# Performance work log

Measured on AMD Instinct MI355X. Metric: run time of the kernel, lower is better.

The kernel has to match this reference:

```python
import jax, jax.numpy as jnp
import numpy as np

NUM_HEADS = 16
NUM_FEATURES = 1024
HEAD_DIM = NUM_FEATURES // NUM_HEADS
B, S = 2, 2048


def setup_inputs() -> dict:
    key = jax.random.key(0)
    ks = jax.random.split(key, 12)
    d = NUM_FEATURES
    scale = 1.0 / np.sqrt(d)
    inp = {
        'q': jax.random.normal(ks[0], (B, S, d), jnp.float32),
        'v': jax.random.normal(ks[1], (B, S, d), jnp.float32),
        'k': jax.random.normal(ks[2], (B, S, d), jnp.float32),
        'mask': jnp.ones((1, 1, S, S), jnp.float32),
        # Dense params: flax kernel layout (in, out)
        'Wq': jax.random.normal(ks[3], (d, d), jnp.float32) * scale,
        'bq': jnp.zeros((d,), jnp.float32),
        'Wv': jax.random.normal(ks[4], (d, d), jnp.float32) * scale,
        'bv': jnp.zeros((d,), jnp.float32),
        'Wk': jax.random.normal(ks[5], (d, d), jnp.float32) * scale,
        'bk': jnp.zeros((d,), jnp.float32),
        'Wo': jax.random.normal(ks[6], (d, d), jnp.float32) * scale,
        'bo': jnp.zeros((d,), jnp.float32),
    }
    return inp


def _split_heads(x):
    b, s, _ = x.shape
    return jnp.transpose(x.reshape(b, s, NUM_HEADS, HEAD_DIM), (0, 2, 1, 3))  # [B,H,S,Dh]


def reference(q, v, k, mask, Wq, bq, Wv, bv, Wk, bk, Wo, bo):
    q = q @ Wq + bq
    v = v @ Wv + bv
    k = k @ Wk + bk
    qh = _split_heads(q) / jnp.sqrt(jnp.float32(NUM_FEATURES))  # note: sqrt(d_model), as in source
    kh = _split_heads(k)
    vh = _split_heads(v)
    logits = jnp.einsum('bhqd,bhkd->bhqk', qh, kh)
    logits = logits - 1e9 * (1.0 - mask)
    weights = jax.nn.softmax(logits, axis=-1)
    # dropout deterministic (eval_mode=True) -> identity
    out = jnp.einsum('bhqk,bhkd->bhqd', weights, vh)
    out = jnp.transpose(out, (0, 2, 1, 3)).reshape(q.shape[0], q.shape[1], NUM_FEATURES)
    return out @ Wo + bo
```

## Files before the change

kernel.cpp:

```cpp
#include <hip/hip_runtime.h>
#include <hip/hip_bf16.h>


namespace {
constexpr int DM = 1024;
constexpr int NH = 16;
constexpr int HD = 64;
constexpr int SQ = 2048;
constexpr int M_TOT = 2 * SQ;
constexpr int NT = SQ / 64;

using f32x4  = __attribute__((ext_vector_type(4))) float;
using f32x16 = __attribute__((ext_vector_type(16))) float;
using bf16x8 = __attribute__((ext_vector_type(8))) short;
using u16 = unsigned short;

__device__ __forceinline__ u16 f2bf(float f) {
  union { float f; unsigned u; } x; x.f = f;
  unsigned r = x.u + 0x7fffu + ((x.u >> 16) & 1u);
  return (u16)(r >> 16);
}

__device__ __forceinline__ unsigned pk2(float lo, float hi) {
  unsigned r;
  asm("v_cvt_pk_bf16_f32 %0, %1, %2" : "=v"(r) : "v"(lo), "v"(hi));
  return r;
}

__device__ __forceinline__ float fexp2(float x) {
  float r;
  asm("v_exp_f32 %0, %1" : "=v"(r) : "v"(x));
  return r;
}

__device__ __forceinline__ f32x16 mfma32(bf16x8 a, bf16x8 b, f32x16 c) {
  return __builtin_amdgcn_mfma_f32_32x32x16_bf16(a, b, c, 0, 0, 0);
}

__device__ __forceinline__ void gld16(const void* g, void* l) {
  __builtin_amdgcn_global_load_lds((const __attribute__((address_space(1))) void*)g,
                                   (__attribute__((address_space(3))) void*)l, 16, 0, 0);
}
}

__global__ __launch_bounds__(256) void tobf_kernel(const float* __restrict__ q,
                                                   const float* __restrict__ k,
                                                   const float* __restrict__ v,
                                                   u16* __restrict__ out) {
  const float* src = blockIdx.y == 0 ? q : (blockIdx.y == 1 ? k : v);
  u16* dst = out + (size_t)blockIdx.y * M_TOT * DM;
  size_t i = ((size_t)blockIdx.x * 256 + threadIdx.x) * 8;
  float4 a = *(const float4*)(src + i), b = *(const float4*)(src + i + 4);
  union { u16 us[8]; uint4 v4; } pk;
  pk.us[0] = f2bf(a.x); pk.us[1] = f2bf(a.y); pk.us[2] = f2bf(a.z); pk.us[3] = f2bf(a.w);
  pk.us[4] = f2bf(b.x); pk.us[5] = f2bf(b.y); pk.us[6] = f2bf(b.z); pk.us[7] = f2bf(b.w);
  *(uint4*)(dst + i) = pk.v4;
}

__global__ __launch_bounds__(256) void wtrans_kernel(const float* __restrict__ W,
                                                     u16* __restrict__ Wt) {
  __shared__ u16 tile[64][65];
  const int t = threadIdx.x;
  const int k0 = blockIdx.y * 64, n0 = blockIdx.x * 64;
#pragma unroll
  for (int i = 0; i < 16; ++i) {
    int flat = t + i * 256;
    int kk = flat >> 6, nn = flat & 63;
    tile[kk][nn] = f2bf(W[(size_t)(k0 + kk) * DM + n0 + nn]);
  }
  __syncthreads();
#pragma unroll
  for (int i = 0; i < 16; ++i) {
    int flat = t + i * 256;
    int nn = flat >> 6, kk = flat & 63;
    Wt[(size_t)(n0 + nn) * DM + k0 + kk] = tile[kk][nn];
  }
}

__global__ __launch_bounds__(256) void vtrans_kernel(const u16* __restrict__ Vh,
                                                     u16* __restrict__ Vt) {
  __shared__ u16 tile[64][80];
  const int s0 = blockIdx.x * 64, bh = blockIdx.y;
  const u16* src = Vh + ((size_t)bh * SQ + s0) * HD;
  u16* dst = Vt + (size_t)bh * HD * SQ + s0;
  const int t = threadIdx.x;
#pragma unroll
  for (int i = 0; i < 2; ++i) {
    int flat = t + i * 256;
    int sr = flat >> 3, ch = flat & 7;
    *(uint4*)&tile[sr][ch * 8] = *(const uint4*)&src[(size_t)sr * HD + ch * 8];
  }
  __syncthreads();
#pragma unroll
  for (int i = 0; i < 2; ++i) {
    int flat = t + i * 256;
    int dh = flat >> 3, ch = flat & 7;
    union { u16 us[8]; uint2 h[2]; } pk;
#pragma unroll
    for (int j = 0; j < 8; ++j) pk.us[j] = tile[ch * 8 + j][dh];
#pragma unroll
    for (int kq = 0; kq < 2; ++kq) {
      int g = ch * 2 + kq;
      int gl = (g & ~3) | ((g & 1) << 1) | ((g & 2) >> 1);
      *(uint2*)&dst[(size_t)dh * SQ + gl * 4] = pk.h[kq];
    }
  }
}

template <int EPI>
__device__ __forceinline__ void gemm_core(const u16* __restrict__ A,
                                          const u16* __restrict__ Wt,
                                          const float* __restrict__ bias,
                                          void* __restrict__ C, float scale,
                                          int m0, int n0, u16* ldsA, u16* ldsB) {
  const int t = threadIdx.x;
  const int lane = t & 63, w = t >> 6;
  const int wm = w >> 1, wn = w & 1;
  const int c = lane & 15, g = lane >> 4;
  const int lr = lane >> 3, lc = lane & 7;
  f32x4 acc[2][4] = {};

  for (int k0 = 0; k0 < DM; k0 += 64) {
    __syncthreads();
#pragma unroll
    for (int j = 0; j < 2; ++j) {
      int row = w * 16 + j * 8 + lr;
      int gc = lc ^ (row & 7);
      gld16(&A[(size_t)(m0 + row) * DM + k0 + gc * 8], (char*)ldsA + w * 2048 + j * 1024);
    }
#pragma unroll
    for (int j = 0; j < 4; ++j) {
      int row = w * 32 + j * 8 + lr;
      int gc = lc ^ (row & 7);
      gld16(&Wt[(size_t)(n0 + row) * DM + k0 + gc * 8], (char*)ldsB + w * 4096 + j * 1024);
    }
    __syncthreads();
#pragma unroll
    for (int ks = 0; ks < 2; ++ks) {
      bf16x8 af[2], bfr[4];
#pragma unroll
      for (int mi = 0; mi < 2; ++mi) {
        int R = wm * 32 + mi * 16 + c;
        af[mi] = *(const bf16x8*)((const char*)ldsA + R * 128 + ((4 * ks + g) ^ (R & 7)) * 16);
      }
#pragma unroll
      for (int ni = 0; ni < 4; ++ni) {
        int R = wn * 64 + ni * 16 + c;
        bfr[ni] = *(const bf16x8*)((const char*)ldsB + R * 128 + ((4 * ks + g) ^ (R & 7)) * 16);
      }
#pragma unroll
      for (int mi = 0; mi < 2; ++mi)
#pragma unroll
        for (int ni = 0; ni < 4; ++ni)
          acc[mi][ni] =
              __builtin_amdgcn_mfma_f32_16x16x32_bf16(af[mi], bfr[ni], acc[mi][ni], 0, 0, 0);
    }
  }
  float bv_[4];
#pragma unroll
  for (int ni = 0; ni < 4; ++ni) bv_[ni] = bias[n0 + wn * 64 + ni * 16 + c];
#pragma unroll
  for (int mi = 0; mi < 2; ++mi)
#pragma unroll
    for (int ni = 0; ni < 4; ++ni)
#pragma unroll
      for (int r = 0; r < 4; ++r) {
        int m = m0 + wm * 32 + mi * 16 + g * 4 + r;
        int n = n0 + wn * 64 + ni * 16 + c;
        float val = acc[mi][ni][r] + bv_[ni];
        if (EPI == 2) {
          ((float*)C)[(size_t)m * DM + n] = val;
        } else {
          int b = m >> 11, s = m & (SQ - 1);
          int h = n >> 6, dh = n & (HD - 1);
          ((u16*)C)[((size_t)(b * NH + h) * SQ + s) * HD + dh] = f2bf(val * scale);
        }
      }
}

__global__ __launch_bounds__(256) void qkvgemm_kernel(const u16* __restrict__ QKVbf,
                                                      const u16* __restrict__ W3t,
                                                      const float* __restrict__ bq,
                                                      const float* __restrict__ bk,
                                                      const float* __restrict__ bv,
                                                      u16* __restrict__ Qh,
                                                      u16* __restrict__ Kh,
                                                      u16* __restrict__ Vh) {
  __shared__ __align__(16) u16 ldsA[64 * 64];
  __shared__ __align__(16) u16 ldsB[128 * 64];
  int bid = blockIdx.x;
  int swz = (bid & 7) * 192 + (bid >> 3);
  int which = swz >> 9;
  int sub = swz & 511;
  int mt = sub >> 3, nt = sub & 7;
  const u16* A = QKVbf + (size_t)which * M_TOT * DM;
  const u16* Wt = W3t + (size_t)which * DM * DM;
  const float* bias = which == 0 ? bq : (which == 1 ? bk : bv);
  u16* C = which == 0 ? Qh : (which == 1 ? Kh : Vh);
  float scale = which == 0 ? 0.045084222f : 1.0f;
  gemm_core<0>(A, Wt, bias, C, scale, mt * 64, nt * 128, ldsA, ldsB);
}

__global__ __launch_bounds__(256) void ogemm_kernel(const u16* __restrict__ Ob,
                                                    const u16* __restrict__ Wot,
                                                    const float* __restrict__ bo,
                                                    float* __restrict__ out) {
  __shared__ __align__(16) u16 ldsA[64 * 64];
  __shared__ __align__(16) u16 ldsB[128 * 64];
  int bid = blockIdx.x;
  int swz = (bid & 7) * 64 + (bid >> 3);
  int mt = swz >> 3, nt = swz & 7;
  gemm_core<2>(Ob, Wot, bo, out, 1.0f, mt * 64, nt * 128, ldsA, ldsB);
}

__global__ __launch_bounds__(256) void fattn_kernel(const u16* __restrict__ Qh,
                                                    const u16* __restrict__ Kh,
                                                    const u16* __restrict__ Vt,
                                                    u16* __restrict__ Ob) {
  __shared__ __align__(16) u16 ldsKV[4][2][64 * 64];
  const int t = threadIdx.x;
  const int lane = t & 63, w = t >> 6;
  const int l31 = lane & 31, hi = lane >> 5;

  const int bid = blockIdx.x;
  const int swz = (bid & 7) * 64 + (bid >> 3);
  const int bh = swz >> 4, qb = swz & 15;
  const int q0 = qb * 128 + w * 32;
  const u16* Qb = Qh + (size_t)bh * SQ * HD;
  const u16* Kb = Kh + (size_t)bh * SQ * HD;
  const u16* Vb = Vt + (size_t)bh * HD * SQ;

  bf16x8 qf[4];
#pragma unroll
  for (int ks = 0; ks < 4; ++ks)
    qf[ks] = *(const bf16x8*)&Qb[(size_t)(q0 + l31) * HD + ks * 16 + hi * 8];

  f32x16 o0 = {}, o1 = {};
  float m_run = -3e38f, l_run = 0.f;

  auto stage = [&](int kt, int buf) {
#pragma unroll
    for (int j = 0; j < 2; ++j) {
      int r = j * 32 + w * 8 + (lane >> 3);
      int cg = (lane & 7) ^ (r & 7);
      gld16(&Kb[(size_t)(kt * 64 + r) * HD + cg * 8],
            (char*)&ldsKV[buf][0][0] + j * 4096 + w * 1024);
      gld16(&Vb[(size_t)r * SQ + kt * 64 + cg * 8],
            (char*)&ldsKV[buf][1][0] + j * 4096 + w * 1024);
    }
  };

  auto qk = [&](int kt, f32x16& d0, f32x16& d1) {
    const char* kbp = (const char*)&ldsKV[kt & 3][0][0];
    d0 = (f32x16){};
    d1 = (f32x16){};
#pragma unroll
    for (int ks = 0; ks < 4; ++ks) {
      int ch = ((ks * 2 + hi) ^ (l31 & 7)) * 16;
      bf16x8 k0 = *(const bf16x8*)(kbp + l31 * 128 + ch);
      bf16x8 k1 = *(const bf16x8*)(kbp + (32 + l31) * 128 + ch);
      d0 = mfma32(k0, qf[ks], d0);
      d1 = mfma32(k1, qf[ks], d1);
    }
  };

  auto smpv = [&](int kt, f32x16& s0, f32x16& s1) {
    float mx[16];
#pragma unroll
    for (int r = 0; r < 16; ++r) mx[r] = fmaxf(s0[r], s1[r]);
#pragma unroll
    for (int d = 8; d >= 1; d >>= 1)
#pragma unroll
      for (int r = 0; r < d; ++r) mx[r] = fmaxf(mx[r], mx[r + d]);
    float pmax = fmaxf(mx[0], __shfl_xor(mx[0], 32));
    if (__any(pmax > m_run + 8.0f)) {
      float mnew = fmaxf(m_run, pmax);
      float scf = fexp2(m_run - mnew);
      m_run = mnew;
      l_run *= scf;
#pragma unroll
      for (int r = 0; r < 16; ++r) {
        float sv = __shfl(scf, (r & 3) + 8 * (r >> 2) + 4 * hi);
        o0[r] *= sv;
        o1[r] *= sv;
      }
    }
#pragma unroll
    for (int r = 0; r < 16; ++r) {
      s0[r] = fexp2(s0[r] - m_run);
      s1[r] = fexp2(s1[r] - m_run);
    }
    float sm[16];
#pragma unroll
    for (int r = 0; r < 16; ++r) sm[r] = s0[r] + s1[r];
#pragma unroll
    for (int d = 8; d >= 1; d >>= 1)
#pragma unroll
      for (int r = 0; r < d; ++r) sm[r] += sm[r + d];
    l_run += sm[0];
    union W8 { unsigned u[4]; bf16x8 v; };
    W8 pa[4];
#pragma unroll
    for (int wd = 0; wd < 4; ++wd) {
      pa[0].u[wd] = pk2(s0[2 * wd], s0[2 * wd + 1]);
      pa[1].u[wd] = pk2(s0[8 + 2 * wd], s0[9 + 2 * wd]);
      pa[2].u[wd] = pk2(s1[2 * wd], s1[2 * wd + 1]);
      pa[3].u[wd] = pk2(s1[8 + 2 * wd], s1[9 + 2 * wd]);
    }
    const char* vbp = (const char*)&ldsKV[kt & 3][1][0];
#pragma unroll
    for (int g = 0; g < 4; ++g) {
      int ch = ((g * 2 + hi) ^ (l31 & 7)) * 16;
      bf16x8 v0 = *(const bf16x8*)(vbp + l31 * 128 + ch);
      bf16x8 v1 = *(const bf16x8*)(vbp + (32 + l31) * 128 + ch);
      o0 = mfma32(pa[g].v, v0, o0);
      o1 = mfma32(pa[g].v, v1, o1);
    }
  };

  stage(0, 0);
  stage(1, 1);
  __syncthreads();

  f32x16 sA0, sA1, sB0, sB1;
  qk(0, sA0, sA1);

  for (int it = 0; it < NT / 2 - 1; ++it) {
    const int kt = 2 * it + 1;
    stage(kt + 1, (kt + 1) & 3);
    qk(kt, sB0, sB1);
    smpv(kt - 1, sA0, sA1);
    __syncthreads();
    stage(kt + 2, (kt + 2) & 3);
    qk(kt + 1, sA0, sA1);
    smpv(kt, sB0, sB1);
    __syncthreads();
  }
  qk(NT - 1, sB0, sB1);
  smpv(NT - 2, sA0, sA1);
  smpv(NT - 1, sB0, sB1);

  float l_tot = l_run + __shfl_xor(l_run, 32);
  float linv = 1.0f / l_tot;
  const int b = bh >> 4, h = bh & (NH - 1);
#pragma unroll
  for (int r = 0; r < 16; ++r) {
    int qrow = (r & 3) + 8 * (r >> 2) + 4 * hi;
    float lv = __shfl(linv, qrow);
    size_t base = ((size_t)b * SQ + (q0 + qrow)) * DM + h * HD + l31;
    Ob[base] = f2bf(o0[r] * lv);
    Ob[base + 32] = f2bf(o1[r] * lv);
  }
}

extern "C" void kernel_launch(void* const* d_in, const int* in_sizes, int n_in,
                              void* d_out, int out_size, void* d_ws, size_t ws_size,
                              hipStream_t stream) {
  (void)in_sizes; (void)n_in; (void)out_size; (void)ws_size;
  const float* q  = (const float*)d_in[0];
  const float* v  = (const float*)d_in[1];
  const float* k  = (const float*)d_in[2];
  const float* Wq = (const float*)d_in[4];
  const float* bq = (const float*)d_in[5];
  const float* Wv = (const float*)d_in[6];
  const float* bv = (const float*)d_in[7];
  const float* Wk = (const float*)d_in[8];
  const float* bk = (const float*)d_in[9];
  const float* Wo = (const float*)d_in[10];
  const float* bo = (const float*)d_in[11];

  char* ws = (char*)d_ws;
  const size_t MB = 1024 * 1024;
  u16* W3t   = (u16*)(ws + 0 * MB);
  u16* Wot   = (u16*)(ws + 6 * MB);
  u16* QKVbf = (u16*)(ws + 8 * MB);
  u16* Vh    = (u16*)(ws + 32 * MB);
  u16* Vt    = (u16*)(ws + 8 * MB);
  u16* Ob    = (u16*)(ws + 16 * MB);
  u16* Qh    = (u16*)d_out;
  u16* Kh    = (u16*)d_out + (size_t)4 * 1024 * 1024;

  const dim3 blk(256);
  tobf_kernel<<<dim3(2048, 3), blk, 0, stream>>>(q, k, v, QKVbf);

  const dim3 wtGrid(16, 16);
  wtrans_kernel<<<wtGrid, blk, 0, stream>>>(Wq, W3t);
  wtrans_kernel<<<wtGrid, blk, 0, stream>>>(Wk, W3t + (size_t)DM * DM);
  wtrans_kernel<<<wtGrid, blk, 0, stream>>>(Wv, W3t + (size_t)2 * DM * DM);
  wtrans_kernel<<<wtGrid, blk, 0, stream>>>(Wo, Wot);

  qkvgemm_kernel<<<dim3(1536), blk, 0, stream>>>(QKVbf, W3t, bq, bk, bv, Qh, Kh, Vh);

  vtrans_kernel<<<dim3(32, 32), blk, 0, stream>>>(Vh, Vt);

  fattn_kernel<<<dim3(512), blk, 0, stream>>>(Qh, Kh, Vt, Ob);

  ogemm_kernel<<<dim3(512), blk, 0, stream>>>(Ob, Wot, bo, (float*)d_out);
}
```

Baseline: 131.2 us.

## Split attention keys across two wave groups and merge softmax partials in LDS

```diff
diff --git a/kernel.cpp b/kernel.cpp
--- a/kernel.cpp
+++ b/kernel.cpp
@@ -8,7 +8,6 @@
 constexpr int HD = 64;
 constexpr int SQ = 2048;
 constexpr int M_TOT = 2 * SQ;
-constexpr int NT = SQ / 64;
 
 using f32x4  = __attribute__((ext_vector_type(4))) float;
 using f32x16 = __attribute__((ext_vector_type(16))) float;
@@ -57,8 +56,15 @@
   *(uint4*)(dst + i) = pk.v4;
 }
 
-__global__ __launch_bounds__(256) void wtrans_kernel(const float* __restrict__ W,
-                                                     u16* __restrict__ Wt) {
+__global__ __launch_bounds__(256) void wtrans4_kernel(const float* __restrict__ Wq,
+                                                      const float* __restrict__ Wk,
+                                                      const float* __restrict__ Wv,
+                                                      const float* __restrict__ Wo,
+                                                      u16* __restrict__ W3t,
+                                                      u16* __restrict__ Wot) {
+  const int z = blockIdx.z;
+  const float* W = z == 0 ? Wq : (z == 1 ? Wk : (z == 2 ? Wv : Wo));
+  u16* Wt = z < 3 ? W3t + (size_t)z * DM * DM : Wot;
   __shared__ u16 tile[64][65];
   const int t = threadIdx.x;
   const int k0 = blockIdx.y * 64, n0 = blockIdx.x * 64;
@@ -213,22 +219,25 @@
   gemm_core<2>(Ob, Wot, bo, out, 1.0f, mt * 64, nt * 128, ldsA, ldsB);
 }
 
-__global__ __launch_bounds__(256) void fattn_kernel(const u16* __restrict__ Qh,
-                                                    const u16* __restrict__ Kh,
-                                                    const u16* __restrict__ Vt,
-                                                    u16* __restrict__ Ob) {
-  __shared__ __align__(16) u16 ldsKV[4][2][64 * 64];
+__global__ __launch_bounds__(512, 4) void fattn_kernel(const u16* __restrict__ Qh,
+                                                       const u16* __restrict__ Kh,
+                                                       const u16* __restrict__ Vt,
+                                                       u16* __restrict__ Ob) {
+  __shared__ __align__(16) u16 ldsKV[2][2][2][64 * 64];
+  __shared__ float ldsML[2][8][32];
   const int t = threadIdx.x;
   const int lane = t & 63, w = t >> 6;
   const int l31 = lane & 31, hi = lane >> 5;
+  const int wq = w >> 1, wk = w & 1;
 
   const int bid = blockIdx.x;
   const int swz = (bid & 7) * 64 + (bid >> 3);
   const int bh = swz >> 4, qb = swz & 15;
-  const int q0 = qb * 128 + w * 32;
+  const int q0 = qb * 128 + wq * 32;
   const u16* Qb = Qh + (size_t)bh * SQ * HD;
   const u16* Kb = Kh + (size_t)bh * SQ * HD;
   const u16* Vb = Vt + (size_t)bh * HD * SQ;
+  const int keybase = wk * (SQ / 2);
 
   bf16x8 qf[4];
 #pragma unroll
@@ -241,30 +250,33 @@
   auto stage = [&](int kt, int buf) {
 #pragma unroll
     for (int j = 0; j < 2; ++j) {
-      int r = j * 32 + w * 8 + (lane >> 3);
+      int r = j * 32 + wq * 8 + (lane >> 3);
       int cg = (lane & 7) ^ (r & 7);
-      gld16(&Kb[(size_t)(kt * 64 + r) * HD + cg * 8],
-            (char*)&ldsKV[buf][0][0] + j * 4096 + w * 1024);
-      gld16(&Vb[(size_t)r * SQ + kt * 64 + cg * 8],
-            (char*)&ldsKV[buf][1][0] + j * 4096 + w * 1024);
+      gld16(&Kb[(size_t)(keybase + kt * 64 + r) * HD + cg * 8],
+            (char*)&ldsKV[wk][buf][0][0] + j * 4096 + wq * 1024);
+      gld16(&Vb[(size_t)r * SQ + keybase + kt * 64 + cg * 8],
+            (char*)&ldsKV[wk][buf][1][0] + j * 4096 + wq * 1024);
     }
   };
 
-  auto qk = [&](int kt, f32x16& d0, f32x16& d1) {
-    const char* kbp = (const char*)&ldsKV[kt & 3][0][0];
-    d0 = (f32x16){};
-    d1 = (f32x16){};
+  stage(0, 0);
+  __syncthreads();
+
+  for (int kt = 0; kt < 16; ++kt) {
+    const int cur = kt & 1;
+    if (kt + 1 < 16) stage(kt + 1, cur ^ 1);
+
+    f32x16 s0 = {}, s1 = {};
+    const char* kbp = (const char*)&ldsKV[wk][cur][0][0];
 #pragma unroll
     for (int ks = 0; ks < 4; ++ks) {
       int ch = ((ks * 2 + hi) ^ (l31 & 7)) * 16;
       bf16x8 k0 = *(const bf16x8*)(kbp + l31 * 128 + ch);
       bf16x8 k1 = *(const bf16x8*)(kbp + (32 + l31) * 128 + ch);
-      d0 = mfma32(k0, qf[ks], d0);
-      d1 = mfma32(k1, qf[ks], d1);
-    }
-  };
-
-  auto smpv = [&](int kt, f32x16& s0, f32x16& s1) {
+      s0 = mfma32(k0, qf[ks], s0);
+      s1 = mfma32(k1, qf[ks], s1);
+    }
+
     float mx[16];
 #pragma unroll
     for (int r = 0; r < 16; ++r) mx[r] = fmaxf(s0[r], s1[r]);
@@ -273,6 +285,7 @@
 #pragma unroll
       for (int r = 0; r < d; ++r) mx[r] = fmaxf(mx[r], mx[r + d]);
     float pmax = fmaxf(mx[0], __shfl_xor(mx[0], 32));
+
     if (__any(pmax > m_run + 8.0f)) {
       float mnew = fmaxf(m_run, pmax);
       float scf = fexp2(m_run - mnew);
@@ -298,6 +311,7 @@
 #pragma unroll
       for (int r = 0; r < d; ++r) sm[r] += sm[r + d];
     l_run += sm[0];
+
     union W8 { unsigned u[4]; bf16x8 v; };
     W8 pa[4];
 #pragma unroll
@@ -307,7 +321,8 @@
       pa[2].u[wd] = pk2(s1[2 * wd], s1[2 * wd + 1]);
       pa[3].u[wd] = pk2(s1[8 + 2 * wd], s1[9 + 2 * wd]);
     }
-    const char* vbp = (const char*)&ldsKV[kt & 3][1][0];
+
+    const char* vbp = (const char*)&ldsKV[wk][cur][1][0];
 #pragma unroll
     for (int g = 0; g < 4; ++g) {
       int ch = ((g * 2 + hi) ^ (l31 & 7)) * 16;
@@ -316,40 +331,42 @@
       o0 = mfma32(pa[g].v, v0, o0);
       o1 = mfma32(pa[g].v, v1, o1);
     }
-  };
-
-  stage(0, 0);
-  stage(1, 1);
+
+    __syncthreads();
+  }
+
+  float l2 = l_run + __shfl_xor(l_run, 32);
+  float (*ldsO)[32][64] = (float(*)[32][64]) & ldsKV[0][0][0][0];
+#pragma unroll
+  for (int r = 0; r < 16; ++r) {
+    int q = (r & 3) + 8 * (r >> 2) + 4 * hi;
+    ldsO[w][q][l31] = o0[r];
+    ldsO[w][q][32 + l31] = o1[r];
+  }
+  if (hi == 0) {
+    ldsML[0][w][l31] = m_run;
+    ldsML[1][w][l31] = l2;
+  }
   __syncthreads();
 
-  f32x16 sA0, sA1, sB0, sB1;
-  qk(0, sA0, sA1);
-
-  for (int it = 0; it < NT / 2 - 1; ++it) {
-    const int kt = 2 * it + 1;
-    stage(kt + 1, (kt + 1) & 3);
-    qk(kt, sB0, sB1);
-    smpv(kt - 1, sA0, sA1);
-    __syncthreads();
-    stage(kt + 2, (kt + 2) & 3);
-    qk(kt + 1, sA0, sA1);
-    smpv(kt, sB0, sB1);
-    __syncthreads();
-  }
-  qk(NT - 1, sB0, sB1);
-  smpv(NT - 2, sA0, sA1);
-  smpv(NT - 1, sB0, sB1);
-
-  float l_tot = l_run + __shfl_xor(l_run, 32);
-  float linv = 1.0f / l_tot;
-  const int b = bh >> 4, h = bh & (NH - 1);
-#pragma unroll
-  for (int r = 0; r < 16; ++r) {
-    int qrow = (r & 3) + 8 * (r >> 2) + 4 * hi;
-    float lv = __shfl(linv, qrow);
-    size_t base = ((size_t)b * SQ + (q0 + qrow)) * DM + h * HD + l31;
-    Ob[base] = f2bf(o0[r] * lv);
-    Ob[base + 32] = f2bf(o1[r] * lv);
+  {
+    const int q = t >> 2;
+    const int dh0 = (t & 3) * 16;
+    const int wA = (q >> 5) * 2;
+    const int ql = q & 31;
+    float m0 = ldsML[0][wA][ql], m1 = ldsML[0][wA + 1][ql];
+    float l0 = ldsML[1][wA][ql], l1 = ldsML[1][wA + 1][ql];
+    float mxv = fmaxf(m0, m1);
+    float f0 = fexp2(m0 - mxv), f1 = fexp2(m1 - mxv);
+    float inv = 1.0f / (l0 * f0 + l1 * f1);
+    union { u16 us[16]; uint4 v4[2]; } pk;
+#pragma unroll
+    for (int j = 0; j < 16; ++j)
+      pk.us[j] = f2bf((ldsO[wA][ql][dh0 + j] * f0 + ldsO[wA + 1][ql][dh0 + j] * f1) * inv);
+    const int b = bh >> 4, h = bh & (NH - 1);
+    size_t base = ((size_t)b * SQ + qb * 128 + q) * DM + h * HD + dh0;
+    *(uint4*)&Ob[base] = pk.v4[0];
+    *(uint4*)&Ob[base + 8] = pk.v4[1];
   }
 }
 
@@ -383,17 +400,13 @@
   const dim3 blk(256);
   tobf_kernel<<<dim3(2048, 3), blk, 0, stream>>>(q, k, v, QKVbf);
 
-  const dim3 wtGrid(16, 16);
-  wtrans_kernel<<<wtGrid, blk, 0, stream>>>(Wq, W3t);
-  wtrans_kernel<<<wtGrid, blk, 0, stream>>>(Wk, W3t + (size_t)DM * DM);
-  wtrans_kernel<<<wtGrid, blk, 0, stream>>>(Wv, W3t + (size_t)2 * DM * DM);
-  wtrans_kernel<<<wtGrid, blk, 0, stream>>>(Wo, Wot);
+  wtrans4_kernel<<<dim3(16, 16, 4), blk, 0, stream>>>(Wq, Wk, Wv, Wo, W3t, Wot);
 
   qkvgemm_kernel<<<dim3(1536), blk, 0, stream>>>(QKVbf, W3t, bq, bk, bv, Qh, Kh, Vh);
 
   vtrans_kernel<<<dim3(32, 32), blk, 0, stream>>>(Vh, Vt);
 
-  fattn_kernel<<<dim3(512), blk, 0, stream>>>(Qh, Kh, Vt, Ob);
+  fattn_kernel<<<dim3(512), dim3(512), 0, stream>>>(Qh, Kh, Vt, Ob);
 
   ogemm_kernel<<<dim3(512), blk, 0, stream>>>(Ob, Wot, bo, (float*)d_out);
 }
```

Result: faster. 125.8 us (-4.1%).
